# Kernel optimization log

Measured on AMD Instinct MI355X. Metric: run time of the kernel, lower is better.

## Reference

```python
import jax, jax.numpy as jnp
import numpy as np

STRIDES = (8, 16, 32, 64)
NUM_HEADS = 8
G = 4
P = 32
TAU_Z = 2.0
LVL_BASE = 3.0  # stride 8 == 2**3 maps to level 0


def decode_box(xyzr):
    scale = jnp.exp2(xyzr[..., 2:3])
    ratio = jnp.exp2(jnp.concatenate([-0.5 * xyzr[..., 3:4], 0.5 * xyzr[..., 3:4]], axis=-1))
    wh = scale * ratio
    xy = xyzr[..., 0:2]
    return jnp.concatenate([xy - 0.5 * wh, xy + 0.5 * wh], axis=-1)


def position_embedding(box, num_feats, temperature=10000.0):
    term = jnp.array([1000.0, 1000.0, 1.0, 1.0], dtype=box.dtype)
    token = box / term
    dim_t = jnp.arange(num_feats, dtype=jnp.float32)
    dim_t = temperature ** (2.0 * (dim_t // 2) / num_feats)
    pos = token[..., None] / dim_t  # B,N,4,F
    pos = jnp.stack([jnp.sin(pos[..., 0::2]), jnp.cos(pos[..., 1::2])], axis=4)
    B, N = box.shape[:2]
    return pos.reshape(B, N, -1)  # B,N,4*F


def bbox_iof(boxes):
    # boxes: B,N,4 x1y1x2y2; iof[b,i,j] = inter(i,j) / area(i)
    area = jnp.clip(boxes[..., 2] - boxes[..., 0], 0.0) * jnp.clip(boxes[..., 3] - boxes[..., 1], 0.0)
    lt = jnp.maximum(boxes[:, :, None, :2], boxes[:, None, :, :2])
    rb = jnp.minimum(boxes[:, :, None, 2:], boxes[:, None, :, 2:])
    wh = jnp.clip(rb - lt, 0.0)
    inter = wh[..., 0] * wh[..., 1]
    return inter / jnp.clip(area[:, :, None], 1e-7, None)


def bilinear_group_sample(feat, xy, stride):
    # feat: [B,C,H,W]; xy: [B,N,P,G,2] image coords -> [B,N,G,P,C//G]
    B, C, H, W = feat.shape
    _, N, Pn, Gn, _ = xy.shape
    Cg = C // Gn
    featg = feat.reshape(B, Gn, Cg, H * W).transpose(0, 1, 3, 2)  # B,G,HW,Cg
    px = xy[..., 0] / stride - 0.5  # grid_sample align_corners=False convention
    py = xy[..., 1] / stride - 0.5
    x0 = jnp.floor(px)
    y0 = jnp.floor(py)
    bi = jnp.arange(B)[:, None, None]
    gi = jnp.arange(Gn)[None, :, None]
    out = jnp.zeros((B, Gn, N * Pn, Cg), dtype=feat.dtype)
    for dx in (0.0, 1.0):
        for dy in (0.0, 1.0):
            xi = x0 + dx
            yi = y0 + dy
            wgt = (1.0 - jnp.abs(px - xi)) * (1.0 - jnp.abs(py - yi))
            valid = (xi >= 0) & (xi <= W - 1) & (yi >= 0) & (yi <= H - 1)
            wgt = wgt * valid  # zero padding outside
            xi_c = jnp.clip(xi, 0, W - 1).astype(jnp.int32)
            yi_c = jnp.clip(yi, 0, H - 1).astype(jnp.int32)
            idx = (yi_c * W + xi_c).transpose(0, 3, 1, 2).reshape(B, Gn, N * Pn)
            vals = featg[bi, gi, idx]  # B,G,N*P,Cg
            w = wgt.transpose(0, 3, 1, 2).reshape(B, Gn, N * Pn, 1)
            out = out + vals * w
    return out.reshape(B, Gn, N, Pn, Cg).transpose(0, 2, 1, 3, 4)


def layer_norm(x, g, b, eps=1e-5):
    mu = jnp.mean(x, axis=-1, keepdims=True)
    var = jnp.mean((x - mu) ** 2, axis=-1, keepdims=True)
    return (x - mu) * jax.lax.rsqrt(var + eps) * g + b


def _forward(feats, query_content, query_box, Wq, bq, Wk, bk, Wv, bv, Wo, bo,
             ln_g, ln_b, off_W, off_b, sc_W, sc_b, iof_tau):
    B, N, C = query_content.shape
    H = NUM_HEADS
    dh = C // H
    box_cxcy = query_box[..., :2]
    zc = query_box[..., 2:3]
    rc = query_box[..., 3:4]
    box_wh = jnp.exp2(zc) * jnp.exp2(jnp.concatenate([-0.5 * rc, 0.5 * rc], axis=-1))
    logscale = zc.reshape(B, N, 1, 1)

    # torch.no_grad() block -> stop_gradient
    rois = decode_box(query_box)
    iof = jnp.log(bbox_iof(jax.lax.stop_gradient(rois)) + 1e-7)  # B,N,N
    pe = jax.lax.stop_gradient(position_embedding(query_box, C // 4))  # B,N,C
    attn_bias = iof[:, None, :, :] * iof_tau.reshape(1, -1, 1, 1)  # B,H,N,N

    x = query_content + pe
    q = (x @ Wq.T + bq).reshape(B, N, H, dh)
    k = (x @ Wk.T + bk).reshape(B, N, H, dh)
    v = (x @ Wv.T + bv).reshape(B, N, H, dh)
    scores = jnp.einsum('bnhd,bmhd->bhnm', q, k) * (dh ** -0.5) + attn_bias
    attn = jax.nn.softmax(scores, axis=-1)
    ctx = jnp.einsum('bhnm,bmhd->bnhd', attn, v).reshape(B, N, C)
    qc = x + ctx @ Wo.T + bo  # mmcv MultiheadAttention adds identity (= query+pe)
    qc = layer_norm(qc, ln_g, ln_b)

    offset = (qc @ off_W.T + off_b).reshape(B, N, P, G, 2)
    scale_logit = (qc @ sc_W.T + sc_b).reshape(B, N, P, G)
    sample_xy = box_cxcy.reshape(B, N, 1, 1, 2) + offset * box_wh.reshape(B, N, 1, 1, 2)
    sample_z = scale_logit + logscale  # B,N,P,G
    lvl = sample_z - LVL_BASE
    levels = jnp.arange(len(STRIDES), dtype=jnp.float32)
    zw = jax.nn.softmax(-((lvl[..., None] - levels) ** 2) / TAU_Z, axis=-1)  # B,N,P,G,L
    zw_t = zw.transpose(0, 1, 3, 2, 4)  # B,N,G,P,L
    sample_feats = jnp.zeros(())
    for l, (fm, s) in enumerate(zip(feats, STRIDES)):
        sample_feats = sample_feats + bilinear_group_sample(fm, sample_xy, s) * zw_t[..., l:l + 1]
    return sample_feats, sample_xy, offset, sample_z, scale_logit, qc


def setup_inputs():
    key = jax.random.key(0)
    ks = jax.random.split(key, 20)
    B, N, C = 4, 500, 256
    feat0 = jax.random.normal(ks[0], (B, C, 128, 128), dtype=jnp.float32)
    feat1 = jax.random.normal(ks[1], (B, C, 64, 64), dtype=jnp.float32)
    feat2 = jax.random.normal(ks[2], (B, C, 32, 32), dtype=jnp.float32)
    feat3 = jax.random.normal(ks[3], (B, C, 16, 16), dtype=jnp.float32)
    query_content = jax.random.normal(ks[4], (B, N, C), dtype=jnp.float32)
    xy = jax.random.uniform(ks[5], (B, N, 2), minval=64.0, maxval=960.0)
    zz = jax.random.uniform(ks[6], (B, N, 1), minval=3.0, maxval=6.0)
    rr = jax.random.uniform(ks[7], (B, N, 1), minval=-1.0, maxval=1.0)
    query_box = jnp.concatenate([xy, zz, rr], axis=-1)
    sub_query_xy = jax.random.normal(ks[8], (B, N, P, G, 2), dtype=jnp.float32) * 0.1
    sub_query_z = jax.random.normal(ks[9], (B, N, P, G, 4), dtype=jnp.float32) * 0.1
    sub_query_vec = jax.random.normal(ks[10], (B, N, P, G, 64), dtype=jnp.float32) * 0.1
    imgs_whwh = jnp.full((B, N, 4), 1024.0, dtype=jnp.float32)
    w = lambda i, sh: jax.random.normal(ks[i], sh, dtype=jnp.float32) * 0.02
    return {
        'feat0': feat0, 'feat1': feat1, 'feat2': feat2, 'feat3': feat3,
        'query_content': query_content, 'query_box': query_box,
        'sub_query_xy': sub_query_xy, 'sub_query_z': sub_query_z,
        'sub_query_vec': sub_query_vec, 'imgs_whwh': imgs_whwh,
        'Wq': w(11, (C, C)), 'bq': jnp.zeros((C,), jnp.float32),
        'Wk': w(12, (C, C)), 'bk': jnp.zeros((C,), jnp.float32),
        'Wv': w(13, (C, C)), 'bv': jnp.zeros((C,), jnp.float32),
        'Wo': w(14, (C, C)), 'bo': jnp.zeros((C,), jnp.float32),
        'ln_g': jnp.ones((C,), jnp.float32), 'ln_b': jnp.zeros((C,), jnp.float32),
        'off_W': w(15, (2 * G * P, C)),
        'off_b': jax.random.uniform(ks[16], (2 * G * P,), minval=-0.5, maxval=0.5),
        'sc_W': w(17, (G * P, C)),
        'sc_b': jax.random.normal(ks[18], (G * P,), dtype=jnp.float32) * 0.1,
        'iof_tau': jax.random.uniform(ks[19], (NUM_HEADS,), minval=0.0, maxval=4.0),
    }


def reference(feat0, feat1, feat2, feat3, query_content, query_box, sub_query_xy,
              sub_query_z, sub_query_vec, imgs_whwh, Wq, bq, Wk, bk, Wv, bv, Wo, bo,
              ln_g, ln_b, off_W, off_b, sc_W, sc_b, iof_tau):
    sample_feats, sample_xy, offset, sample_z, scale_logit, qc = _forward(
        [feat0, feat1, feat2, feat3], query_content, query_box,
        Wq, bq, Wk, bk, Wv, bv, Wo, bo, ln_g, ln_b, off_W, off_b, sc_W, sc_b, iof_tau)
    return (sample_feats, sub_query_xy, sub_query_z, sub_query_vec, qc,
            sample_xy, offset, sample_z, scale_logit)
```

## Files before the change

### kernel.cpp

```cpp
#include <hip/hip_runtime.h>
#include <cstdint>
#include <cstddef>

#define B_ 4
#define N_ 500
#define C_ 256
#define NH_ 8
#define DH_ 32
#define P_ 32
#define G_ 4
#define CG_ 64
#define BN_ (B_*N_)
#define QKV_QI 8

__constant__ const int LVL_W[4] = {128, 64, 32, 16};

static __device__ __forceinline__ unsigned short f2bf(float f) {
  union { float f; unsigned u; } v; v.f = f;
  unsigned r = v.u + 0x7FFF + ((v.u >> 16) & 1);
  return (unsigned short)(r >> 16);
}
static __device__ __forceinline__ float bf2f(unsigned u16shifted) {
  union { unsigned u; float f; } v; v.u = u16shifted;
  return v.f;
}

__global__ __launch_bounds__(256) void mega_kernel(
    const float* __restrict__ f0, const float* __restrict__ f1,
    const float* __restrict__ f2, const float* __restrict__ f3,
    unsigned short* __restrict__ t0, unsigned short* __restrict__ t1,
    unsigned short* __restrict__ t2, unsigned short* __restrict__ t3) {
  __shared__ unsigned short tile[64][260];
  int blk = blockIdx.x;
  int t = threadIdx.x;
  const float* src; unsigned short* dst; int npix, i;
  if (blk < 1024)      { src = f0; dst = t0; npix = 16384; i = blk; }
  else if (blk < 1280) { src = f1; dst = t1; npix = 4096;  i = blk - 1024; }
  else if (blk < 1344) { src = f2; dst = t2; npix = 1024;  i = blk - 1280; }
  else                 { src = f3; dst = t3; npix = 256;   i = blk - 1344; }
  int pb = npix >> 8;
  int px0 = (i % pb) * 256;
  int c0 = ((i / pb) & 3) * 64;
  int b  = i / (pb * 4);
  int lane = t & 63;
  int wv = t >> 6;
#pragma unroll
  for (int k = 0; k < 16; k++) {
    int r = k * 4 + wv;
    float4 v = *(const float4*)&src[((size_t)b * C_ + c0 + r) * npix + px0 + lane * 4];
    ushort4 u;
    u.x = f2bf(v.x); u.y = f2bf(v.y); u.z = f2bf(v.z); u.w = f2bf(v.w);
    int col = (lane * 4) ^ (((r >> 4) & 3) << 2);
    *(ushort4*)&tile[r][col] = u;
  }
  __syncthreads();
  int cq = t & 15;
  int pr = t >> 4;
#pragma unroll
  for (int k = 0; k < 16; k++) {
    int p = k * 16 + pr;
    ushort4 r4;
    {
      int ch = cq * 4;
      r4.x = tile[ch + 0][p ^ ((((ch + 0) >> 4) & 3) << 2)];
      r4.y = tile[ch + 1][p ^ ((((ch + 1) >> 4) & 3) << 2)];
      r4.z = tile[ch + 2][p ^ ((((ch + 2) >> 4) & 3) << 2)];
      r4.w = tile[ch + 3][p ^ ((((ch + 3) >> 4) & 3) << 2)];
    }
    *(ushort4*)&dst[((size_t)b * npix + px0 + p) * C_ + c0 + cq * 4] = r4;
  }
}

__global__ __launch_bounds__(256) void qkv_prep_kernel(
    const float* __restrict__ qcontent, const float* __restrict__ qbox,
    const float* __restrict__ Wq, const float* __restrict__ bq,
    const float* __restrict__ Wk, const float* __restrict__ bk,
    const float* __restrict__ Wv, const float* __restrict__ bv,
    float* __restrict__ x, float* __restrict__ boxd,
    float* __restrict__ q, float* __restrict__ kT, float* __restrict__ vT) {
  __shared__ float xs[QKV_QI][C_];
  int blk = blockIdx.x;
  int t = threadIdx.x;
  int bn0 = blk * QKV_QI;
  int d = t >> 6;
  float tj = exp2f((float)((t >> 1) & 31) * 0.4152410f);
  float tmul = (d < 2) ? 0.001f : 1.0f;
  for (int i = 0; i < QKV_QI; i++) {
    float qv = qbox[(size_t)(bn0 + i) * 4 + d];
    float val = qv * tmul / tj;
    float pe = (t & 1) ? cosf(val) : sinf(val);
    float xv = qcontent[(size_t)(bn0 + i) * C_ + t] + pe;
    xs[i][t] = xv;
    x[(size_t)(bn0 + i) * C_ + t] = xv;
  }
  if (t < QKV_QI) {
    int bn = bn0 + t;
    const float* qb = qbox + (size_t)bn * 4;
    float cx = qb[0], cy = qb[1], z = qb[2], r = qb[3];
    float scale = exp2f(z);
    float w = scale * exp2f(-0.5f * r);
    float h = scale * exp2f(0.5f * r);
    float* bd = boxd + (size_t)bn * 12;
    float x1 = cx - 0.5f * w, y1 = cy - 0.5f * h, x2 = cx + 0.5f * w, y2 = cy + 0.5f * h;
    bd[0] = x1; bd[1] = y1; bd[2] = x2; bd[3] = y2;
    bd[4] = cx; bd[5] = cy; bd[6] = w; bd[7] = h; bd[8] = z;
    float area = fmaxf(x2 - x1, 0.f) * fmaxf(y2 - y1, 0.f);
    bd[9] = fmaxf(area, 1e-7f);
  }
  __syncthreads();
  float accq[QKV_QI], acck[QKV_QI], accv[QKV_QI];
  for (int i = 0; i < QKV_QI; i++) { accq[i] = 0.f; acck[i] = 0.f; accv[i] = 0.f; }
  const float4* wq4 = (const float4*)(Wq + (size_t)t * C_);
  const float4* wk4 = (const float4*)(Wk + (size_t)t * C_);
  const float4* wv4 = (const float4*)(Wv + (size_t)t * C_);
  for (int k4 = 0; k4 < C_ / 4; k4++) {
    float4 wq = wq4[k4], wk = wk4[k4], wv = wv4[k4];
    for (int i = 0; i < QKV_QI; i++) {
      float4 xv = *(const float4*)&xs[i][k4 * 4];
      accq[i] += xv.x * wq.x + xv.y * wq.y + xv.z * wq.z + xv.w * wq.w;
      acck[i] += xv.x * wk.x + xv.y * wk.y + xv.z * wk.z + xv.w * wk.w;
      accv[i] += xv.x * wv.x + xv.y * wv.y + xv.z * wv.z + xv.w * wv.w;
    }
  }
  for (int i = 0; i < QKV_QI; i++) {
    int bn = bn0 + i;
    int b = bn / N_;
    int n = bn % N_;
    q[(size_t)bn * C_ + t] = accq[i] + bq[t];
    kT[((size_t)b * C_ + t) * N_ + n] = acck[i] + bk[t];
    vT[((size_t)b * C_ + t) * N_ + n] = accv[i] + bv[t];
  }
}

__global__ __launch_bounds__(256) void score_copy_kernel(
    const float* __restrict__ q, const float* __restrict__ kT,
    const float* __restrict__ boxd, const float* __restrict__ tau_p,
    float* __restrict__ S, float* __restrict__ Mpart,
    const float* __restrict__ subxy, const float* __restrict__ subz,
    const float* __restrict__ subv,
    float* __restrict__ o_subxy, float* __restrict__ o_subz,
    float* __restrict__ o_subv) {
  int blk = blockIdx.x;
  int t = threadIdx.x;
  if (blk >= 512) {
    int cb = blk - 512;
    const float4* s4; float4* d4;
    if (cb < 125)      { s4 = (const float4*)subxy + (size_t)cb * 1024;
                         d4 = (float4*)o_subxy + (size_t)cb * 1024; }
    else if (cb < 375) { s4 = (const float4*)subz + (size_t)(cb - 125) * 1024;
                         d4 = (float4*)o_subz + (size_t)(cb - 125) * 1024; }
    else               { s4 = (const float4*)subv + (size_t)(cb - 375) * 1024;
                         d4 = (float4*)o_subv + (size_t)(cb - 375) * 1024; }
    d4[t] = s4[t];
    d4[t + 256] = s4[t + 256];
    d4[t + 512] = s4[t + 512];
    d4[t + 768] = s4[t + 768];
    return;
  }
  int mp = (blk >> 1) & 7;
  int npar = blk & 1;
  int h = (blk >> 4) & 7;
  int b = blk >> 7;
  int w = t >> 6;
  int lane = t & 63;
  int m = mp * 64 + lane;
  int mc = min(m, N_ - 1);
  bool mok = m < N_;
  float tau = tau_p[h];
  const float scl = 0.17677669529663687f;

  float kreg[DH_];
  const float* kbase = kT + ((size_t)b * C_ + h * DH_) * N_ + mc;
#pragma unroll
  for (int d = 0; d < DH_; d++) kreg[d] = kbase[(size_t)d * N_];

  const float* bm = boxd + ((size_t)b * N_ + mc) * 12;
  float kx1 = bm[0], ky1 = bm[1], kx2 = bm[2], ky2 = bm[3];

  size_t srow_base = ((size_t)(b * NH_ + h)) * N_;
  for (int n = npar * 4 + w; n < N_; n += 8) {
    const float* qn = q + ((size_t)b * N_ + n) * C_ + h * DH_;
    float4 q0 = *(const float4*)&qn[0];
    float4 q1 = *(const float4*)&qn[4];
    float4 q2 = *(const float4*)&qn[8];
    float4 q3 = *(const float4*)&qn[12];
    float4 q4 = *(const float4*)&qn[16];
    float4 q5 = *(const float4*)&qn[20];
    float4 q6 = *(const float4*)&qn[24];
    float4 q7 = *(const float4*)&qn[28];
    float s0 = q0.x*kreg[0] + q0.y*kreg[1] + q0.z*kreg[2] + q0.w*kreg[3];
    float s1 = q1.x*kreg[4] + q1.y*kreg[5] + q1.z*kreg[6] + q1.w*kreg[7];
    float s2 = q2.x*kreg[8] + q2.y*kreg[9] + q2.z*kreg[10] + q2.w*kreg[11];
    float s3 = q3.x*kreg[12] + q3.y*kreg[13] + q3.z*kreg[14] + q3.w*kreg[15];
    s0 += q4.x*kreg[16] + q4.y*kreg[17] + q4.z*kreg[18] + q4.w*kreg[19];
    s1 += q5.x*kreg[20] + q5.y*kreg[21] + q5.z*kreg[22] + q5.w*kreg[23];
    s2 += q6.x*kreg[24] + q6.y*kreg[25] + q6.z*kreg[26] + q6.w*kreg[27];
    s3 += q7.x*kreg[28] + q7.y*kreg[29] + q7.z*kreg[30] + q7.w*kreg[31];
    float s = (s0 + s1) + (s2 + s3);

    const float* bn = boxd + ((size_t)b * N_ + n) * 12;
    float4 nb = *(const float4*)&bn[0];
    float inv_area = 1.0f / bn[9];
    float iw = fmaxf(fminf(nb.z, kx2) - fmaxf(nb.x, kx1), 0.f);
    float ih = fmaxf(fminf(nb.w, ky2) - fmaxf(nb.y, ky1), 0.f);
    float bias = logf(iw * ih * inv_area + 1e-7f);
    float sc = s * scl + bias * tau;

    if (mok) S[(srow_base + n) * 512 + m] = sc;
    float wm = mok ? sc : -1e30f;
#pragma unroll
    for (int off = 32; off >= 1; off >>= 1) wm = fmaxf(wm, __shfl_xor(wm, off, 64));
    if (lane == 0) Mpart[(srow_base + n) * 8 + mp] = wm;
  }
}

__global__ __launch_bounds__(256) void pv_kernel(
    const float* __restrict__ S, const float* __restrict__ Mpart,
    const float* __restrict__ vT, float* __restrict__ ctx) {
  int w = threadIdx.x >> 6;
  int lane = threadIdx.x & 63;
  int n0 = blockIdx.x * 4;
  int h = blockIdx.y * 4 + w;
  int b = blockIdx.z;
  size_t rb = ((size_t)(b * NH_ + h)) * N_;

  float mval = -1e30f;
  if (lane < 32) mval = Mpart[(rb + n0 + (lane >> 3)) * 8 + (lane & 7)];
  mval = fmaxf(mval, __shfl_xor(mval, 1, 64));
  mval = fmaxf(mval, __shfl_xor(mval, 2, 64));
  mval = fmaxf(mval, __shfl_xor(mval, 4, 64));
  float mx[4];
#pragma unroll
  for (int n = 0; n < 4; n++) mx[n] = __shfl(mval, n * 8, 64);

  float p[4][8];
  float inv[4];
#pragma unroll
  for (int n = 0; n < 4; n++) {
    const float* Srow = S + (rb + n0 + n) * 512;
    float sum = 0.f;
#pragma unroll
    for (int i = 0; i < 8; i++) {
      int m = lane + 64 * i;
      float sv = Srow[min(m, N_ - 1)];
      float e = (m < N_) ? __expf(sv - mx[n]) : 0.f;
      p[n][i] = e;
      sum += e;
    }
#pragma unroll
    for (int off = 32; off >= 1; off >>= 1) sum += __shfl_xor(sum, off, 64);
    inv[n] = 1.0f / sum;
  }

  const float* vbase = vT + ((size_t)b * C_ + h * DH_) * N_;
  float keep0 = 0.f, keep1 = 0.f, keep2 = 0.f, keep3 = 0.f;
  for (int cc = 0; cc < DH_; cc++) {
    const float* vrow = vbase + (size_t)cc * N_;
    float a0 = 0.f, a1 = 0.f, a2 = 0.f, a3 = 0.f;
#pragma unroll
    for (int i = 0; i < 8; i++) {
      int m = lane + 64 * i;
      float vv = vrow[min(m, N_ - 1)];
      a0 += p[0][i] * vv;
      a1 += p[1][i] * vv;
      a2 += p[2][i] * vv;
      a3 += p[3][i] * vv;
    }
#pragma unroll
    for (int off = 32; off >= 1; off >>= 1) {
      a0 += __shfl_xor(a0, off, 64);
      a1 += __shfl_xor(a1, off, 64);
      a2 += __shfl_xor(a2, off, 64);
      a3 += __shfl_xor(a3, off, 64);
    }
    bool sel = (lane & 31) == cc;
    keep0 = sel ? a0 : keep0;
    keep1 = sel ? a1 : keep1;
    keep2 = sel ? a2 : keep2;
    keep3 = sel ? a3 : keep3;
  }
  int c = lane & 31;
  size_t obase = ((size_t)b * N_ + n0) * C_ + h * DH_ + c;
  if (lane < 32) {
    ctx[obase + 0 * C_] = keep0 * inv[0];
    ctx[obase + 2 * C_] = keep2 * inv[2];
  } else {
    ctx[obase + 1 * C_] = keep1 * inv[1];
    ctx[obase + 3 * C_] = keep3 * inv[3];
  }
}

#define PQI 4
__global__ __launch_bounds__(256) void projln_head_kernel(
    const float* __restrict__ ctx, const float* __restrict__ x,
    const float* __restrict__ Wo, const float* __restrict__ bo,
    const float* __restrict__ ln_g, const float* __restrict__ ln_b,
    const float* __restrict__ boxd,
    const float* __restrict__ offW, const float* __restrict__ offb,
    const float* __restrict__ scW, const float* __restrict__ scb,
    float* __restrict__ qc_out,
    float* __restrict__ out_offset, float* __restrict__ out_sxy,
    float* __restrict__ out_sz, float* __restrict__ out_sl,
    float* __restrict__ zw_ws) {
  __shared__ float cs[PQI][C_];
  __shared__ float qs[PQI][C_];
  __shared__ float redbuf[PQI][8];
  int blk = blockIdx.x;
  int t = threadIdx.x;
  int bn0 = blk * PQI;
  for (int i = 0; i < PQI; i++) cs[i][t] = ctx[(size_t)(bn0 + i) * C_ + t];
  __syncthreads();
  float acc[PQI] = {0.f, 0.f, 0.f, 0.f};
  {
    const float4* w4 = (const float4*)(Wo + (size_t)t * C_);
    for (int k4 = 0; k4 < C_ / 4; k4++) {
      float4 w = w4[k4];
      for (int i = 0; i < PQI; i++) {
        float4 cv = *(const float4*)&cs[i][k4 * 4];
        acc[i] += cv.x * w.x + cv.y * w.y + cv.z * w.z + cv.w * w.w;
      }
    }
  }
  float y[PQI];
  int wave = t >> 6, lane = t & 63;
  for (int i = 0; i < PQI; i++) {
    y[i] = x[(size_t)(bn0 + i) * C_ + t] + acc[i] + bo[t];
    float s1 = y[i], s2 = y[i] * y[i];
#pragma unroll
    for (int off = 32; off >= 1; off >>= 1) {
      s1 += __shfl_xor(s1, off, 64);
      s2 += __shfl_xor(s2, off, 64);
    }
    if (lane == 0) { redbuf[i][wave] = s1; redbuf[i][wave + 4] = s2; }
  }
  __syncthreads();
  for (int i = 0; i < PQI; i++) {
    float s1 = redbuf[i][0] + redbuf[i][1] + redbuf[i][2] + redbuf[i][3];
    float s2 = redbuf[i][4] + redbuf[i][5] + redbuf[i][6] + redbuf[i][7];
    float mu = s1 * (1.0f / C_);
    float var = s2 * (1.0f / C_) - mu * mu;
    float inv = rsqrtf(var + 1e-5f);
    float o = (y[i] - mu) * inv * ln_g[t] + ln_b[t];
    qs[i][t] = o;
    qc_out[(size_t)(bn0 + i) * C_ + t] = o;
  }
  __syncthreads();
  float ao[PQI] = {0.f, 0.f, 0.f, 0.f};
  {
    const float4* w4 = (const float4*)(offW + (size_t)t * C_);
    for (int k4 = 0; k4 < C_ / 4; k4++) {
      float4 w = w4[k4];
      for (int i = 0; i < PQI; i++) {
        float4 cv = *(const float4*)&qs[i][k4 * 4];
        ao[i] += cv.x * w.x + cv.y * w.y + cv.z * w.z + cv.w * w.w;
      }
    }
  }
  int xy = t & 1;
  for (int i = 0; i < PQI; i++) {
    int bn = bn0 + i;
    const float* bd = boxd + (size_t)bn * 12;
    float off = ao[i] + offb[t];
    float ctr = xy ? bd[5] : bd[4];
    float wh = xy ? bd[7] : bd[6];
    float sxy = ctr + off * wh;
    out_offset[(size_t)bn * 256 + t] = off;
    out_sxy[(size_t)bn * 256 + t] = sxy;
  }
  if (t < 128) {
    float as[PQI] = {0.f, 0.f, 0.f, 0.f};
    const float4* sw4 = (const float4*)(scW + (size_t)t * C_);
    for (int k4 = 0; k4 < C_ / 4; k4++) {
      float4 w = sw4[k4];
      for (int i = 0; i < PQI; i++) {
        float4 cv = *(const float4*)&qs[i][k4 * 4];
        as[i] += cv.x * w.x + cv.y * w.y + cv.z * w.z + cv.w * w.w;
      }
    }
    for (int i = 0; i < PQI; i++) {
      int bn = bn0 + i;
      const float* bd = boxd + (size_t)bn * 12;
      float sl = as[i] + scb[t];
      float sz = sl + bd[8];
      out_sl[(size_t)bn * 128 + t] = sl;
      out_sz[(size_t)bn * 128 + t] = sz;
      float lvl = sz - 3.0f;
      float d1 = lvl - 1.f, d2 = lvl - 2.f, d3 = lvl - 3.f;
      float e0 = __expf(-0.5f * lvl * lvl);
      float e1 = __expf(-0.5f * d1 * d1);
      float e2 = __expf(-0.5f * d2 * d2);
      float e3 = __expf(-0.5f * d3 * d3);
      float inv = 1.0f / (e0 + e1 + e2 + e3);
      float* zw = zw_ws + ((size_t)bn * 128 + t) * 4;
      zw[0] = e0 * inv; zw[1] = e1 * inv; zw[2] = e2 * inv; zw[3] = e3 * inv;
    }
  }
}

__global__ __launch_bounds__(256) void sample_kernel_v4(
    const unsigned short* __restrict__ f0, const unsigned short* __restrict__ f1,
    const unsigned short* __restrict__ f2, const unsigned short* __restrict__ f3,
    const float* __restrict__ sxy, const float* __restrict__ zw_ws,
    float* __restrict__ out) {
  int t = threadIdx.x;
  int wv = t >> 6;
  int lane = t & 63;
  int sub = lane >> 3;
  int c8 = lane & 7;
  int pt = blockIdx.x * 32 + wv * 8 + sub;
  int g = pt & 3;
  int p = (pt >> 2) & 31;
  int bn = pt >> 7;
  int b = bn / N_;

  float sx = sxy[(size_t)pt * 2];
  float sy = sxy[(size_t)pt * 2 + 1];
  const float* zw = zw_ws + (size_t)pt * 4;
  const unsigned short* feats[4] = {f0, f1, f2, f3};
  const float inv_stride[4] = {0.125f, 0.0625f, 0.03125f, 0.015625f};
  float acc0 = 0.f, acc1 = 0.f, acc2 = 0.f, acc3 = 0.f;
  float acc4 = 0.f, acc5 = 0.f, acc6 = 0.f, acc7 = 0.f;
#pragma unroll
  for (int l = 0; l < 4; l++) {
    float wl = zw[l];
    int W = LVL_W[l];
    float px = sx * inv_stride[l] - 0.5f;
    float py = sy * inv_stride[l] - 0.5f;
    float x0f = floorf(px), y0f = floorf(py);
    float fx = px - x0f, fy = py - y0f;
    int x0 = (int)x0f, y0 = (int)y0f;
    const unsigned short* fb = feats[l] + (size_t)b * W * W * C_ + g * CG_ + c8 * 8;
#pragma unroll
    for (int dy = 0; dy < 2; dy++) {
#pragma unroll
      for (int dx = 0; dx < 2; dx++) {
        int xi = x0 + dx, yi = y0 + dy;
        float valid = (xi >= 0 && xi < W && yi >= 0 && yi < W) ? 1.f : 0.f;
        int xc = min(max(xi, 0), W - 1);
        int yc = min(max(yi, 0), W - 1);
        float wgt = (dx ? fx : 1.f - fx) * (dy ? fy : 1.f - fy) * valid * wl;
        uint4 u = *(const uint4*)&fb[((size_t)yc * W + xc) * C_];
        acc0 += wgt * bf2f(u.x << 16);
        acc1 += wgt * bf2f(u.x & 0xFFFF0000u);
        acc2 += wgt * bf2f(u.y << 16);
        acc3 += wgt * bf2f(u.y & 0xFFFF0000u);
        acc4 += wgt * bf2f(u.z << 16);
        acc5 += wgt * bf2f(u.z & 0xFFFF0000u);
        acc6 += wgt * bf2f(u.w << 16);
        acc7 += wgt * bf2f(u.w & 0xFFFF0000u);
      }
    }
  }
  float* ob = &out[(size_t)bn * 8192 + g * 2048 + p * 64 + c8 * 8];
  float4 o0 = {acc0, acc1, acc2, acc3};
  float4 o1 = {acc4, acc5, acc6, acc7};
  *(float4*)&ob[0] = o0;
  *(float4*)&ob[4] = o1;
}

__global__ __launch_bounds__(256) void sample_kernel_native(
    const float* __restrict__ f0, const float* __restrict__ f1,
    const float* __restrict__ f2, const float* __restrict__ f3,
    const float* __restrict__ sxy, const float* __restrict__ zw_ws,
    float* __restrict__ out) {
  int t = threadIdx.x;
  int wv = t >> 6;
  int lane = t & 63;
  int pt = blockIdx.x * 4 + wv;
  int g = pt & 3;
  int p = (pt >> 2) & 31;
  int bn = pt >> 7;
  int b = bn / N_;
  float sx = sxy[(size_t)pt * 2];
  float sy = sxy[(size_t)pt * 2 + 1];
  const float* zw = zw_ws + (size_t)pt * 4;
  const float* feats[4] = {f0, f1, f2, f3};
  const float inv_stride[4] = {0.125f, 0.0625f, 0.03125f, 0.015625f};
  float acc = 0.f;
#pragma unroll
  for (int l = 0; l < 4; l++) {
    float wl = zw[l];
    int W = LVL_W[l];
    float px = sx * inv_stride[l] - 0.5f;
    float py = sy * inv_stride[l] - 0.5f;
    float x0f = floorf(px), y0f = floorf(py);
    float fx = px - x0f, fy = py - y0f;
    int x0 = (int)x0f, y0 = (int)y0f;
#pragma unroll
    for (int dy = 0; dy < 2; dy++) {
#pragma unroll
      for (int dx = 0; dx < 2; dx++) {
        int xi = x0 + dx, yi = y0 + dy;
        if (xi >= 0 && xi < W && yi >= 0 && yi < W) {
          float wgt = (dx ? fx : 1.f - fx) * (dy ? fy : 1.f - fy);
          float v = feats[l][(((size_t)b * C_ + g * CG_ + lane) * W + yi) * W + xi];
          acc += wgt * wl * v;
        }
      }
    }
  }
  out[(size_t)bn * 8192 + g * 2048 + p * 64 + lane] = acc;
}

extern "C" void kernel_launch(void* const* d_in, const int* in_sizes, int n_in,
                              void* d_out, int out_size, void* d_ws, size_t ws_size,
                              hipStream_t stream) {
  (void)in_sizes; (void)n_in; (void)out_size;
  const float* feat[4] = {(const float*)d_in[0], (const float*)d_in[1],
                          (const float*)d_in[2], (const float*)d_in[3]};
  const float* query_content = (const float*)d_in[4];
  const float* query_box = (const float*)d_in[5];
  const float* Wq = (const float*)d_in[10]; const float* bq = (const float*)d_in[11];
  const float* Wk = (const float*)d_in[12]; const float* bk = (const float*)d_in[13];
  const float* Wv = (const float*)d_in[14]; const float* bv = (const float*)d_in[15];
  const float* Wo = (const float*)d_in[16]; const float* bo = (const float*)d_in[17];
  const float* ln_g = (const float*)d_in[18]; const float* ln_b = (const float*)d_in[19];
  const float* offW = (const float*)d_in[20]; const float* offb = (const float*)d_in[21];
  const float* scW = (const float*)d_in[22]; const float* scb = (const float*)d_in[23];
  const float* iof_tau = (const float*)d_in[24];

  float* out = (float*)d_out;
  float* ws = (float*)d_ws;

  const size_t O_FEATS = 0;
  const size_t O_SUBXY = 16384000;
  const size_t O_SUBZ = 16896000;
  const size_t O_SUBV = 17920000;
  const size_t O_QC = 34304000;
  const size_t O_SXY = 34816000;
  const size_t O_OFF = 35328000;
  const size_t O_SZ = 35840000;
  const size_t O_SL = 36096000;

  float* S = out + O_FEATS;
  float* Mpart = out + O_FEATS + 8192000;

  const size_t o_x = 0;
  const size_t o_boxd = o_x + 512000;
  const size_t o_q = o_boxd + 24000;
  const size_t o_kT = o_q + 512000;
  const size_t o_vT = o_kT + 512000;
  const size_t o_ctx = o_vT + 512000;
  const size_t o_zw = o_ctx + 512000;
  const size_t o_ft = o_zw + 1024000;
  const size_t ft_sz[4] = {16777216, 4194304, 1048576, 262144};
  const size_t ft_total = ft_sz[0] + ft_sz[1] + ft_sz[2] + ft_sz[3];
  const size_t need_T = o_ft * sizeof(float) + ft_total * sizeof(unsigned short);
  const bool useT = ws_size >= need_T;

  unsigned short* ftu = (unsigned short*)(ws + o_ft);
  unsigned short* ftb[4] = {ftu,
                            ftu + ft_sz[0],
                            ftu + ft_sz[0] + ft_sz[1],
                            ftu + ft_sz[0] + ft_sz[1] + ft_sz[2]};

  if (useT) {
    mega_kernel<<<1360, 256, 0, stream>>>(
        feat[0], feat[1], feat[2], feat[3],
        ftb[0], ftb[1], ftb[2], ftb[3]);
  }

  qkv_prep_kernel<<<BN_ / QKV_QI, 256, 0, stream>>>(
      query_content, query_box, Wq, bq, Wk, bk, Wv, bv,
      ws + o_x, ws + o_boxd, ws + o_q, ws + o_kT, ws + o_vT);

  score_copy_kernel<<<512 + 4375, 256, 0, stream>>>(
      ws + o_q, ws + o_kT, ws + o_boxd, iof_tau, S, Mpart,
      (const float*)d_in[6], (const float*)d_in[7], (const float*)d_in[8],
      out + O_SUBXY, out + O_SUBZ, out + O_SUBV);

  {
    dim3 gb(N_ / 4, 2, B_);
    pv_kernel<<<gb, 256, 0, stream>>>(S, Mpart, ws + o_vT, ws + o_ctx);
  }

  projln_head_kernel<<<BN_ / PQI, 256, 0, stream>>>(
      ws + o_ctx, ws + o_x, Wo, bo, ln_g, ln_b, ws + o_boxd,
      offW, offb, scW, scb,
      out + O_QC, out + O_OFF, out + O_SXY, out + O_SZ, out + O_SL,
      ws + o_zw);

  const int npoints = BN_ * P_ * G_;
  if (useT) {
    sample_kernel_v4<<<npoints / 32, 256, 0, stream>>>(
        ftb[0], ftb[1], ftb[2], ftb[3],
        out + O_SXY, ws + o_zw, out + O_FEATS);
  } else {
    sample_kernel_native<<<npoints / 4, 256, 0, stream>>>(
        feat[0], feat[1], feat[2], feat[3],
        out + O_SXY, ws + o_zw, out + O_FEATS);
  }
}
```

Measured before the change: 287.3 us.

## Store V row-major and rewrite PV kernel with shared-memory probabilities

The QKV kernel now writes V in row-major [B,N,C] layout instead of transposed, and the attention-value kernel is rewritten so each block handles one head and four queries. Softmax probabilities are staged in shared memory, and each lane accumulates one channel over half the keys. This replaces the old per-channel cross-lane shuffle reductions with coalesced loads of V rows. The trade-off is a 4x larger grid and a block-wide sync, and each block re-reads its head's V slice per 4-query group.

```diff
diff --git a/kernel.cpp b/kernel.cpp
--- a/kernel.cpp
+++ b/kernel.cpp
@@ -77,7 +77,7 @@
     const float* __restrict__ Wk, const float* __restrict__ bk,
     const float* __restrict__ Wv, const float* __restrict__ bv,
     float* __restrict__ x, float* __restrict__ boxd,
-    float* __restrict__ q, float* __restrict__ kT, float* __restrict__ vT) {
+    float* __restrict__ q, float* __restrict__ kT, float* __restrict__ v) {
   __shared__ float xs[QKV_QI][C_];
   int blk = blockIdx.x;
   int t = threadIdx.x;
@@ -128,7 +128,7 @@
     int n = bn % N_;
     q[(size_t)bn * C_ + t] = accq[i] + bq[t];
     kT[((size_t)b * C_ + t) * N_ + n] = acck[i] + bk[t];
-    vT[((size_t)b * C_ + t) * N_ + n] = accv[i] + bv[t];
+    v[(size_t)bn * C_ + t] = accv[i] + bv[t];
   }
 }
 
@@ -214,79 +214,65 @@
   }
 }
 
-__global__ __launch_bounds__(256) void pv_kernel(
+__global__ __launch_bounds__(256) void pv_kernel2(
     const float* __restrict__ S, const float* __restrict__ Mpart,
-    const float* __restrict__ vT, float* __restrict__ ctx) {
-  int w = threadIdx.x >> 6;
-  int lane = threadIdx.x & 63;
+    const float* __restrict__ v, float* __restrict__ ctx) {
+  __shared__ float pl[4][512];
+  __shared__ float red[4][4];
+  int t = threadIdx.x;
   int n0 = blockIdx.x * 4;
-  int h = blockIdx.y * 4 + w;
+  int h = blockIdx.y;
   int b = blockIdx.z;
   size_t rb = ((size_t)(b * NH_ + h)) * N_;
 
-  float mval = -1e30f;
-  if (lane < 32) mval = Mpart[(rb + n0 + (lane >> 3)) * 8 + (lane & 7)];
-  mval = fmaxf(mval, __shfl_xor(mval, 1, 64));
-  mval = fmaxf(mval, __shfl_xor(mval, 2, 64));
-  mval = fmaxf(mval, __shfl_xor(mval, 4, 64));
   float mx[4];
 #pragma unroll
-  for (int n = 0; n < 4; n++) mx[n] = __shfl(mval, n * 8, 64);
-
-  float p[4][8];
-  float inv[4];
-#pragma unroll
-  for (int n = 0; n < 4; n++) {
-    const float* Srow = S + (rb + n0 + n) * 512;
-    float sum = 0.f;
-#pragma unroll
-    for (int i = 0; i < 8; i++) {
-      int m = lane + 64 * i;
-      float sv = Srow[min(m, N_ - 1)];
-      float e = (m < N_) ? __expf(sv - mx[n]) : 0.f;
-      p[n][i] = e;
-      sum += e;
-    }
-#pragma unroll
-    for (int off = 32; off >= 1; off >>= 1) sum += __shfl_xor(sum, off, 64);
-    inv[n] = 1.0f / sum;
-  }
-
-  const float* vbase = vT + ((size_t)b * C_ + h * DH_) * N_;
-  float keep0 = 0.f, keep1 = 0.f, keep2 = 0.f, keep3 = 0.f;
-  for (int cc = 0; cc < DH_; cc++) {
-    const float* vrow = vbase + (size_t)cc * N_;
-    float a0 = 0.f, a1 = 0.f, a2 = 0.f, a3 = 0.f;
-#pragma unroll
-    for (int i = 0; i < 8; i++) {
-      int m = lane + 64 * i;
-      float vv = vrow[min(m, N_ - 1)];
-      a0 += p[0][i] * vv;
-      a1 += p[1][i] * vv;
-      a2 += p[2][i] * vv;
-      a3 += p[3][i] * vv;
-    }
-#pragma unroll
-    for (int off = 32; off >= 1; off >>= 1) {
-      a0 += __shfl_xor(a0, off, 64);
-      a1 += __shfl_xor(a1, off, 64);
-      a2 += __shfl_xor(a2, off, 64);
-      a3 += __shfl_xor(a3, off, 64);
-    }
-    bool sel = (lane & 31) == cc;
-    keep0 = sel ? a0 : keep0;
-    keep1 = sel ? a1 : keep1;
-    keep2 = sel ? a2 : keep2;
-    keep3 = sel ? a3 : keep3;
-  }
+  for (int qq = 0; qq < 4; qq++) {
+    const float* mp = Mpart + (rb + n0 + qq) * 8;
+    float m0 = fmaxf(fmaxf(mp[0], mp[1]), fmaxf(mp[2], mp[3]));
+    float m1 = fmaxf(fmaxf(mp[4], mp[5]), fmaxf(mp[6], mp[7]));
+    mx[qq] = fmaxf(m0, m1);
+  }
+  float psum[4];
+#pragma unroll
+  for (int qq = 0; qq < 4; qq++) {
+    const float* Srow = S + (rb + n0 + qq) * 512;
+    float e0 = (t < N_) ? __expf(Srow[min(t, N_ - 1)] - mx[qq]) : 0.f;
+    int m1i = t + 256;
+    float e1 = (m1i < N_) ? __expf(Srow[min(m1i, N_ - 1)] - mx[qq]) : 0.f;
+    pl[qq][t] = e0;
+    pl[qq][t + 256] = e1;
+    psum[qq] = e0 + e1;
+  }
+  int wv = t >> 6, lane = t & 63;
+#pragma unroll
+  for (int qq = 0; qq < 4; qq++) {
+    float s = psum[qq];
+#pragma unroll
+    for (int off = 32; off >= 1; off >>= 1) s += __shfl_xor(s, off, 64);
+    if (lane == 0) red[qq][wv] = s;
+  }
+  __syncthreads();
+
   int c = lane & 31;
-  size_t obase = ((size_t)b * N_ + n0) * C_ + h * DH_ + c;
-  if (lane < 32) {
-    ctx[obase + 0 * C_] = keep0 * inv[0];
-    ctx[obase + 2 * C_] = keep2 * inv[2];
-  } else {
-    ctx[obase + 1 * C_] = keep1 * inv[1];
-    ctx[obase + 3 * C_] = keep3 * inv[3];
+  int mh = lane >> 5;
+  const float* vb = v + ((size_t)b * N_) * C_ + h * DH_ + c;
+  const float* prow = pl[wv];
+  int mstart = mh ? 252 : 0;
+  int mend = mh ? 500 : 252;
+  float a0 = 0.f, a1 = 0.f, a2 = 0.f, a3 = 0.f;
+  for (int m = mstart; m < mend; m += 4) {
+    float p0 = prow[m], p1 = prow[m + 1], p2 = prow[m + 2], p3 = prow[m + 3];
+    a0 += p0 * vb[(size_t)m * C_];
+    a1 += p1 * vb[(size_t)(m + 1) * C_];
+    a2 += p2 * vb[(size_t)(m + 2) * C_];
+    a3 += p3 * vb[(size_t)(m + 3) * C_];
+  }
+  float a = (a0 + a1) + (a2 + a3);
+  a += __shfl_xor(a, 32, 64);
+  if (mh == 0) {
+    float inv = 1.0f / (red[wv][0] + red[wv][1] + red[wv][2] + red[wv][3]);
+    ctx[((size_t)b * N_ + n0 + wv) * C_ + h * DH_ + c] = a * inv;
   }
 }
 
@@ -539,8 +525,8 @@
   const size_t o_boxd = o_x + 512000;
   const size_t o_q = o_boxd + 24000;
   const size_t o_kT = o_q + 512000;
-  const size_t o_vT = o_kT + 512000;
-  const size_t o_ctx = o_vT + 512000;
+  const size_t o_v = o_kT + 512000;
+  const size_t o_ctx = o_v + 512000;
   const size_t o_zw = o_ctx + 512000;
   const size_t o_ft = o_zw + 1024000;
   const size_t ft_sz[4] = {16777216, 4194304, 1048576, 262144};
@@ -562,7 +548,7 @@
 
   qkv_prep_kernel<<<BN_ / QKV_QI, 256, 0, stream>>>(
       query_content, query_box, Wq, bq, Wk, bk, Wv, bv,
-      ws + o_x, ws + o_boxd, ws + o_q, ws + o_kT, ws + o_vT);
+      ws + o_x, ws + o_boxd, ws + o_q, ws + o_kT, ws + o_v);
 
   score_copy_kernel<<<512 + 4375, 256, 0, stream>>>(
       ws + o_q, ws + o_kT, ws + o_boxd, iof_tau, S, Mpart,
@@ -570,8 +556,8 @@
       out + O_SUBXY, out + O_SUBZ, out + O_SUBV);
 
   {
-    dim3 gb(N_ / 4, 2, B_);
-    pv_kernel<<<gb, 256, 0, stream>>>(S, Mpart, ws + o_vT, ws + o_ctx);
+    dim3 gb(N_ / 4, NH_, B_);
+    pv_kernel2<<<gb, 256, 0, stream>>>(S, Mpart, ws + o_v, ws + o_ctx);
   }
 
   projln_head_kernel<<<BN_ / PQI, 256, 0, stream>>>(
```

Result: no change. 291.2 us (+1.4%).
